# Kernel optimization log

Hardware: AMD Instinct MI355X
Metric: run time of the kernel (lower is better)

The kernel has to match this reference:

```python
import jax, jax.numpy as jnp
import numpy as np

QMIN, QMAX = -128.0, 127.0  # 8-bit signed activation range


def fq_act(x, s):
    """Fake-quantize activations: clip(round(x/s))*s with straight-through estimator."""
    y = jnp.clip(jnp.round(x / s), QMIN, QMAX) * s
    return x + jax.lax.stop_gradient(y - x)


def fq_weight(w):
    """Per-tensor max-abs symmetric (narrow-range) 8-bit weight fake-quant with STE."""
    s = jnp.max(jnp.abs(w)) / 127.0
    y = jnp.clip(jnp.round(w / s), -127.0, 127.0) * s
    return w + jax.lax.stop_gradient(y - w)


def conv1x1(x, w, b):
    # x: [b,c,h,w], w: [o,c] -> [b,o,h,w]
    return jnp.einsum('bchw,oc->bohw', x, w) + b[None, :, None, None]


def setup_inputs() -> dict:
    key = jax.random.key(0)
    ks = jax.random.split(key, 6)
    B, C, HC, H, W = 8, 64, 32, 64, 64
    x = jax.random.normal(ks[0], (B, C, H, W), dtype=jnp.float32)
    wq = jax.random.normal(ks[1], (HC, C), dtype=jnp.float32) * 0.05
    wk = jax.random.normal(ks[2], (HC, C), dtype=jnp.float32) * 0.05
    wv = jax.random.normal(ks[3], (HC, C), dtype=jnp.float32) * 0.05
    wp = jax.random.normal(ks[4], (C, HC), dtype=jnp.float32) * 0.05
    return {
        'x': x,
        'wq': wq, 'bq': jnp.zeros((HC,), jnp.float32),
        'wk': wk, 'bk': jnp.zeros((HC,), jnp.float32),
        'wv': wv, 'bv': jnp.zeros((HC,), jnp.float32),
        'wp': wp, 'bp': jnp.zeros((C,), jnp.float32),
        's_in': jnp.ones((1,), jnp.float32) * 0.0625,
        's_out': jnp.ones((1,), jnp.float32) * 0.0625,
    }


def reference(x, wq, bq, wk, bk, wv, bv, wp, bp, s_in, s_out):
    b, c, h, w = x.shape
    hc = wq.shape[0]
    n = h * w
    xq = fq_act(x, s_in)                              # quant_inp(x)
    q = conv1x1(xq, fq_weight(wq), bq).reshape(b, hc, n).transpose(0, 2, 1)  # [b,n,hc]
    k = conv1x1(xq, fq_weight(wk), bk).reshape(b, hc, n)                     # [b,hc,n]
    v = conv1x1(xq, fq_weight(wv), bv).reshape(b, hc, n).transpose(0, 2, 1)  # [b,n,hc]
    z = jax.nn.softmax(jnp.einsum('bqc,bck->bqk', q, k), axis=-1)            # [b,n,n]
    z = jnp.einsum('bqk,bkc->bqc', z, v).transpose(0, 2, 1).reshape(b, hc, h, w)
    z = fq_act(z, s_in)                               # quant_inp(z) (shared module/scale)
    out = xq + conv1x1(z, fq_weight(wp), bp)
    return fq_act(out, s_out)                         # self.act QuantIdentity
```

## Files before the change

kernel.cpp:

```cpp
#include <hip/hip_runtime.h>
#include <hip/hip_bf16.h>
#include <cstdint>
#include <cstddef>

#define NB 8
#define NC 64
#define NHC 32
#define NN 4096
#define LOG2E 1.44269504088896340736f

typedef short v8s __attribute__((ext_vector_type(8)));
typedef short v4s __attribute__((ext_vector_type(4)));
typedef float v4f __attribute__((ext_vector_type(4)));
typedef unsigned int v2u __attribute__((ext_vector_type(2)));

__device__ __forceinline__ unsigned short f2b(float f) {
    unsigned int u = __builtin_bit_cast(unsigned int, f);
    u += 0x7fffu + ((u >> 16) & 1u);
    return (unsigned short)(u >> 16);
}
__device__ __forceinline__ float b2f(unsigned short s) {
    unsigned int u = ((unsigned int)s) << 16;
    return __builtin_bit_cast(float, u);
}
__device__ __forceinline__ unsigned int pack2_bf16(float a, float b) {
    unsigned int ua = __builtin_bit_cast(unsigned int, a);
    ua += 0x7fffu + ((ua >> 16) & 1u);
    unsigned int ub = __builtin_bit_cast(unsigned int, b);
    ub += 0x7fffu + ((ub >> 16) & 1u);
    return (ua >> 16) | (ub & 0xffff0000u);
}
__device__ __forceinline__ unsigned int trunc2_bf16(float a, float b) {
    return __builtin_amdgcn_perm(__builtin_bit_cast(unsigned int, b),
                                 __builtin_bit_cast(unsigned int, a), 0x07060302u);
}
__device__ __forceinline__ float wave_max(float v) {
    #pragma unroll
    for (int off = 1; off < 64; off <<= 1) v = fmaxf(v, __shfl_xor(v, off));
    return v;
}
__device__ __forceinline__ v4f mfma16bf16(v4s a, v4s b, v4f c) {
#if __has_builtin(__builtin_amdgcn_mfma_f32_16x16x16bf16_1k)
    return __builtin_amdgcn_mfma_f32_16x16x16bf16_1k(a, b, c, 0, 0, 0);
#else
    asm volatile("v_mfma_f32_16x16x16_bf16 %0, %1, %2, %0"
                 : "+v"(c) : "v"(a), "v"(b));
    return c;
#endif
}

__global__ __launch_bounds__(256) void k_qkv(
    const float* __restrict__ x,
    const float* __restrict__ wq, const float* __restrict__ wk, const float* __restrict__ wv,
    const float* __restrict__ bq, const float* __restrict__ bk, const float* __restrict__ bv,
    const float* __restrict__ s_in,
    unsigned short* __restrict__ xqb, unsigned short* __restrict__ qb,
    unsigned short* __restrict__ kb, unsigned short* __restrict__ vb)
{
    int blk = blockIdx.x;
    int b   = blk >> 6;
    int p0  = (blk & 63) * 64;
    int tid = threadIdx.x;
    int wave = tid >> 6;
    int lane = tid & 63;

    __shared__ __align__(16) unsigned short xt[64][72];
    __shared__ __align__(16) unsigned short wlds[6144];
    __shared__ float red[3][4];

    float4 q0 = *(const float4*)(wq + tid * 8), q1 = *(const float4*)(wq + tid * 8 + 4);
    float4 k0 = *(const float4*)(wk + tid * 8), k1 = *(const float4*)(wk + tid * 8 + 4);
    float4 v0 = *(const float4*)(wv + tid * 8), v1 = *(const float4*)(wv + tid * 8 + 4);
    float mq = fmaxf(fmaxf(fmaxf(fabsf(q0.x), fabsf(q0.y)), fmaxf(fabsf(q0.z), fabsf(q0.w))),
                     fmaxf(fmaxf(fabsf(q1.x), fabsf(q1.y)), fmaxf(fabsf(q1.z), fabsf(q1.w))));
    float mk = fmaxf(fmaxf(fmaxf(fabsf(k0.x), fabsf(k0.y)), fmaxf(fabsf(k0.z), fabsf(k0.w))),
                     fmaxf(fmaxf(fabsf(k1.x), fabsf(k1.y)), fmaxf(fabsf(k1.z), fabsf(k1.w))));
    float mv = fmaxf(fmaxf(fmaxf(fabsf(v0.x), fabsf(v0.y)), fmaxf(fabsf(v0.z), fabsf(v0.w))),
                     fmaxf(fmaxf(fabsf(v1.x), fabsf(v1.y)), fmaxf(fabsf(v1.z), fabsf(v1.w))));
    mq = wave_max(mq); mk = wave_max(mk); mv = wave_max(mv);
    if (lane == 0) { red[0][wave] = mq; red[1][wave] = mk; red[2][wave] = mv; }
    __syncthreads();
    float sq = fmaxf(fmaxf(red[0][0], red[0][1]), fmaxf(red[0][2], red[0][3])) / 127.0f;
    float sk = fmaxf(fmaxf(red[1][0], red[1][1]), fmaxf(red[1][2], red[1][3])) / 127.0f;
    float sw = fmaxf(fmaxf(red[2][0], red[2][1]), fmaxf(red[2][2], red[2][3])) / 127.0f;
    {
        float eq[8] = {q0.x, q0.y, q0.z, q0.w, q1.x, q1.y, q1.z, q1.w};
        float ek[8] = {k0.x, k0.y, k0.z, k0.w, k1.x, k1.y, k1.z, k1.w};
        float ev[8] = {v0.x, v0.y, v0.z, v0.w, v1.x, v1.y, v1.z, v1.w};
        #pragma unroll
        for (int j = 0; j < 8; ++j) {
            wlds[0 * 2048 + tid * 8 + j] = f2b(fminf(fmaxf(rintf(eq[j] / sq), -127.f), 127.f) * sq);
            wlds[1 * 2048 + tid * 8 + j] = f2b(fminf(fmaxf(rintf(ek[j] / sk), -127.f), 127.f) * sk);
            wlds[2 * 2048 + tid * 8 + j] = f2b(fminf(fmaxf(rintf(ev[j] / sw), -127.f), 127.f) * sw);
        }
    }

    float sv = s_in[0];
    float sinv = 1.0f / sv;
    int jj = tid & 15;
    int c0 = tid >> 4;
    #pragma unroll
    for (int it = 0; it < 4; ++it) {
        int c = c0 + it * 16;
        size_t gi = ((size_t)(b * NC + c) << 12) + p0 + jj * 4;
        float4 xv = *(const float4*)(x + gi);
        float r0 = fminf(fmaxf(rintf(xv.x * sinv), -128.f), 127.f) * sv;
        float r1 = fminf(fmaxf(rintf(xv.y * sinv), -128.f), 127.f) * sv;
        float r2 = fminf(fmaxf(rintf(xv.z * sinv), -128.f), 127.f) * sv;
        float r3 = fminf(fmaxf(rintf(xv.w * sinv), -128.f), 127.f) * sv;
        *(uint2*)(xqb + gi) = make_uint2(pack2_bf16(r0, r1), pack2_bf16(r2, r3));
        xt[jj * 4 + 0][c] = f2b(r0);
        xt[jj * 4 + 1][c] = f2b(r1);
        xt[jj * 4 + 2][c] = f2b(r2);
        xt[jj * 4 + 3][c] = f2b(r3);
    }
    __syncthreads();

    int quad = lane >> 4;
    int l15  = lane & 15;

    v8s bf0 = *(const v8s*)(&xt[wave * 16 + l15][0  + quad * 8]);
    v8s bf1 = *(const v8s*)(&xt[wave * 16 + l15][32 + quad * 8]);

    int pos = p0 + wave * 16 + l15;
    size_t posg = (size_t)b * NN + pos;
    int posP = p0 + (l15 >> 2) * 16 + wave * 4 + (l15 & 3);
    const v4f zc = {0.f, 0.f, 0.f, 0.f};

    #pragma unroll
    for (int rb = 0; rb < 6; ++rb) {
        v8s a0 = *(const v8s*)(wlds + (rb * 16 + l15) * 64 + 0  + quad * 8);
        v8s a1 = *(const v8s*)(wlds + (rb * 16 + l15) * 64 + 32 + quad * 8);
        v4f t   = __builtin_amdgcn_mfma_f32_16x16x32_bf16(a0, bf0, zc, 0, 0, 0);
        v4f acc = __builtin_amdgcn_mfma_f32_16x16x32_bf16(a1, bf1, t, 0, 0, 0);

        int R0 = rb * 16 + quad * 4;
        float vals[4];
        #pragma unroll
        for (int r = 0; r < 4; ++r) {
            int R = R0 + r;
            float bias = (R < 32) ? bq[R] : (R < 64) ? bk[R - 32] : bv[R - 64];
            float vv = acc[r] + bias;
            if (R < 32) vv *= LOG2E;
            vals[r] = vv;
        }
        if (R0 < 32) {
            *(unsigned int*)(qb + posg * NHC + R0)     = pack2_bf16(vals[0], vals[1]);
            *(unsigned int*)(qb + posg * NHC + R0 + 2) = pack2_bf16(vals[2], vals[3]);
        } else if (R0 < 64) {
            *(unsigned int*)(kb + posg * NHC + R0 - 32)     = pack2_bf16(vals[0], vals[1]);
            *(unsigned int*)(kb + posg * NHC + R0 - 32 + 2) = pack2_bf16(vals[2], vals[3]);
        } else {
            #pragma unroll
            for (int r = 0; r < 4; ++r)
                vb[(size_t)(b * NHC + R0 - 64 + r) * NN + posP] = f2b(vals[r]);
        }
    }
}

__global__ __launch_bounds__(256, 2) void k_attn(
    const unsigned short* __restrict__ qb, const unsigned short* __restrict__ kb,
    const unsigned short* __restrict__ vb, const unsigned short* __restrict__ xqb,
    const float* __restrict__ wp, const float* __restrict__ bp,
    const float* __restrict__ s_in, const float* __restrict__ s_out,
    float* __restrict__ out)
{
    int blk  = blockIdx.x;
    int b    = blk >> 6;
    int qt   = blk & 63;
    int qbase = qt * 64;
    int tid  = threadIdx.x;
    int wave = tid >> 6;
    int lane = tid & 63;
    int quad = lane >> 4;
    int l15  = lane & 15;

    __shared__ __align__(16) float zbuf[4][64][36];
    __shared__ float lbuf[4][64];
    __shared__ __align__(16) unsigned short wpq[2048];
    __shared__ float redw[4];

    {
        float4 a0 = *(const float4*)(wp + tid * 8), a1 = *(const float4*)(wp + tid * 8 + 4);
        float mx = fmaxf(fmaxf(fmaxf(fabsf(a0.x), fabsf(a0.y)), fmaxf(fabsf(a0.z), fabsf(a0.w))),
                         fmaxf(fmaxf(fabsf(a1.x), fabsf(a1.y)), fmaxf(fabsf(a1.z), fabsf(a1.w))));
        mx = wave_max(mx);
        if (lane == 0) redw[wave] = mx;
        __syncthreads();
        float scale = fmaxf(fmaxf(redw[0], redw[1]), fmaxf(redw[2], redw[3])) / 127.0f;
        float e[8] = {a0.x, a0.y, a0.z, a0.w, a1.x, a1.y, a1.z, a1.w};
        #pragma unroll
        for (int j = 0; j < 8; ++j) {
            float r = fminf(fmaxf(rintf(e[j] / scale), -127.f), 127.f);
            wpq[tid * 8 + j] = f2b(r * scale);
        }
    }

    const unsigned short* qbat = qb + (size_t)b * NN * NHC;
    const unsigned short* kbat = kb + (size_t)b * NN * NHC;
    const unsigned short* vbat = vb + (size_t)b * NHC * NN;

    v8s qf[4];
    #pragma unroll
    for (int s = 0; s < 4; ++s)
        qf[s] = *(const v8s*)(qbat + (qbase + s * 16 + l15) * NHC + quad * 8);

    const v4f zc = {0.f, 0.f, 0.f, 0.f};
    v4f zt[4][2] = {{zc, zc}, {zc, zc}, {zc, zc}, {zc, zc}};
    float psA[4] = {0.f, 0.f, 0.f, 0.f};
    float psB[4] = {0.f, 0.f, 0.f, 0.f};

    int k0 = wave * 1024;
    const unsigned short* vrow0 = vbat + (size_t)( 0 + l15) * NN;
    const unsigned short* vrow1 = vbat + (size_t)(16 + l15) * NN;

    v8s ck0 = *(const v8s*)(kbat + (k0 +  0 + l15) * NHC + quad * 8);
    v8s ck1 = *(const v8s*)(kbat + (k0 + 16 + l15) * NHC + quad * 8);
    v8s ck2 = *(const v8s*)(kbat + (k0 + 32 + l15) * NHC + quad * 8);
    v8s ck3 = *(const v8s*)(kbat + (k0 + 48 + l15) * NHC + quad * 8);

    #pragma unroll 1
    for (int i = 0; i < 16; ++i) {
        int cki = k0 + (i << 6);
        int nki = k0 + (((i + 1) & 15) << 6);
        v8s nk0 = *(const v8s*)(kbat + (nki +  0 + l15) * NHC + quad * 8);
        v8s nk1 = *(const v8s*)(kbat + (nki + 16 + l15) * NHC + quad * 8);
        v8s nk2 = *(const v8s*)(kbat + (nki + 32 + l15) * NHC + quad * 8);
        v8s nk3 = *(const v8s*)(kbat + (nki + 48 + l15) * NHC + quad * 8);
        v8s v00 = *(const v8s*)(vrow0 + cki + quad * 16);
        v8s v01 = *(const v8s*)(vrow0 + cki + quad * 16 + 8);
        v8s v10 = *(const v8s*)(vrow1 + cki + quad * 16);
        v8s v11 = *(const v8s*)(vrow1 + cki + quad * 16 + 8);
        v4s va[2][4];
        va[0][0] = __builtin_shufflevector(v00, v00, 0, 1, 2, 3);
        va[0][1] = __builtin_shufflevector(v00, v00, 4, 5, 6, 7);
        va[0][2] = __builtin_shufflevector(v01, v01, 0, 1, 2, 3);
        va[0][3] = __builtin_shufflevector(v01, v01, 4, 5, 6, 7);
        va[1][0] = __builtin_shufflevector(v10, v10, 0, 1, 2, 3);
        va[1][1] = __builtin_shufflevector(v10, v10, 4, 5, 6, 7);
        va[1][2] = __builtin_shufflevector(v11, v11, 0, 1, 2, 3);
        va[1][3] = __builtin_shufflevector(v11, v11, 4, 5, 6, 7);

        #pragma unroll
        for (int s = 0; s < 4; ++s) {
            v4f sa[4];
            sa[0] = __builtin_amdgcn_mfma_f32_16x16x32_bf16(ck0, qf[s], zc, 0, 0, 0);
            sa[1] = __builtin_amdgcn_mfma_f32_16x16x32_bf16(ck1, qf[s], zc, 0, 0, 0);
            sa[2] = __builtin_amdgcn_mfma_f32_16x16x32_bf16(ck2, qf[s], zc, 0, 0, 0);
            sa[3] = __builtin_amdgcn_mfma_f32_16x16x32_bf16(ck3, qf[s], zc, 0, 0, 0);

            #pragma unroll
            for (int t = 0; t < 4; ++t) {
                float p0 = __builtin_amdgcn_exp2f(sa[t][0]);
                float p1 = __builtin_amdgcn_exp2f(sa[t][1]);
                float p2 = __builtin_amdgcn_exp2f(sa[t][2]);
                float p3 = __builtin_amdgcn_exp2f(sa[t][3]);
                psA[s] += p0 + p1;
                psB[s] += p2 + p3;
                v2u w;
                w.x = trunc2_bf16(p0, p1);
                w.y = trunc2_bf16(p2, p3);
                v4s pfrag = __builtin_bit_cast(v4s, w);
                zt[s][0] = mfma16bf16(va[0][t], pfrag, zt[s][0]);
                zt[s][1] = mfma16bf16(va[1][t], pfrag, zt[s][1]);
            }
        }
        ck0 = nk0; ck1 = nk1; ck2 = nk2; ck3 = nk3;
    }

    #pragma unroll
    for (int s = 0; s < 4; ++s) {
        *(v4f*)(&zbuf[wave][s * 16 + l15][     quad * 4]) = zt[s][0];
        *(v4f*)(&zbuf[wave][s * 16 + l15][16 + quad * 4]) = zt[s][1];
        float ps = psA[s] + psB[s];
        ps += __shfl_xor(ps, 16);
        ps += __shfl_xor(ps, 32);
        if (quad == 0) lbuf[wave][s * 16 + l15] = ps;
    }
    __syncthreads();

    int myq = wave * 16 + l15;
    float L = lbuf[0][myq] + lbuf[1][myq] + lbuf[2][myq] + lbuf[3][myq];

    float z[8] = {0.f};
    #pragma unroll
    for (int w = 0; w < 4; ++w) {
        v4f za  = *(const v4f*)(&zbuf[w][myq][quad * 8]);
        v4f zb2 = *(const v4f*)(&zbuf[w][myq][quad * 8 + 4]);
        #pragma unroll
        for (int j = 0; j < 4; ++j) { z[j] += za[j]; z[4 + j] += zb2[j]; }
    }
    float sv = s_in[0], sinv = 1.0f / sv;
    float so = s_out[0], soinv = 1.0f / so;
    float Linv = 1.0f / L;
    unsigned int zp[4];
    #pragma unroll
    for (int jp = 0; jp < 4; ++jp) {
        float a = z[2 * jp]     * Linv;
        float c = z[2 * jp + 1] * Linv;
        a = fminf(fmaxf(rintf(a * sinv), -128.f), 127.f) * sv;
        c = fminf(fmaxf(rintf(c * sinv), -128.f), 127.f) * sv;
        zp[jp] = pack2_bf16(a, c);
    }
    v8s zf = __builtin_bit_cast(v8s, *(uint4*)zp);

    v8s w0f = *(const v8s*)(wpq + ( 0 + l15) * NHC + quad * 8);
    v8s w1f = *(const v8s*)(wpq + (16 + l15) * NHC + quad * 8);
    v8s w2f = *(const v8s*)(wpq + (32 + l15) * NHC + quad * 8);
    v8s w3f = *(const v8s*)(wpq + (48 + l15) * NHC + quad * 8);
    v4f o0 = __builtin_amdgcn_mfma_f32_16x16x32_bf16(w0f, zf, zc, 0, 0, 0);
    v4f o1 = __builtin_amdgcn_mfma_f32_16x16x32_bf16(w1f, zf, zc, 0, 0, 0);
    v4f o2 = __builtin_amdgcn_mfma_f32_16x16x32_bf16(w2f, zf, zc, 0, 0, 0);
    v4f o3 = __builtin_amdgcn_mfma_f32_16x16x32_bf16(w3f, zf, zc, 0, 0, 0);

    int pos = qbase + wave * 16 + l15;
    #pragma unroll
    for (int ot = 0; ot < 4; ++ot) {
        v4f ov = (ot == 0) ? o0 : (ot == 1) ? o1 : (ot == 2) ? o2 : o3;
        #pragma unroll
        for (int r = 0; r < 4; ++r) {
            int oc = ot * 16 + quad * 4 + r;
            size_t idx = (size_t)(b * NC + oc) * NN + pos;
            float val = ov[r] + bp[oc] + b2f(xqb[idx]);
            float f = fminf(fmaxf(rintf(val * soinv), -128.f), 127.f);
            out[idx] = f * so;
        }
    }
}

extern "C" void kernel_launch(void* const* d_in, const int* in_sizes, int n_in,
                              void* d_out, int out_size, void* d_ws, size_t ws_size,
                              hipStream_t stream) {
    const float* x     = (const float*)d_in[0];
    const float* wq    = (const float*)d_in[1];
    const float* bq    = (const float*)d_in[2];
    const float* wk    = (const float*)d_in[3];
    const float* bk    = (const float*)d_in[4];
    const float* wv    = (const float*)d_in[5];
    const float* bv    = (const float*)d_in[6];
    const float* wp    = (const float*)d_in[7];
    const float* bp    = (const float*)d_in[8];
    const float* s_in  = (const float*)d_in[9];
    const float* s_out = (const float*)d_in[10];
    float* out = (float*)d_out;

    char* ws = (char*)d_ws;
    size_t off = 0;
    auto carve = [&](size_t bytes) {
        void* p = ws + off;
        off = (off + bytes + 255) & ~(size_t)255;
        return p;
    };
    unsigned short* xqb = (unsigned short*)carve((size_t)NB * NC * NN * 2);
    unsigned short* qbf = (unsigned short*)carve((size_t)NB * NN * NHC * 2);
    unsigned short* kbf = (unsigned short*)carve((size_t)NB * NN * NHC * 2);
    unsigned short* vbf = (unsigned short*)carve((size_t)NB * NHC * NN * 2);

    hipLaunchKernelGGL(k_qkv, dim3(512), dim3(256), 0, stream,
                       x, wq, wk, wv, bq, bk, bv, s_in, xqb, qbf, kbf, vbf);
    hipLaunchKernelGGL(k_attn, dim3(512), dim3(256), 0, stream,
                       qbf, kbf, vbf, xqb, wp, bp, s_in, s_out, out);
}
```

Baseline: 112.7 us.

## Use 16x16x32 MFMA for PV product with matching V layout and prefetch

Replaces the 16x16x16 bf16 MFMAs in the attention P·V step with 16x16x32 MFMAs that consume two score tiles at once. This halves the PV instruction count and drops the per-iteration shuffles of V fragments. The V store permutation in the QKV kernel changes so each lane's 8 contiguous keys line up with the new fragment layout. V fragments are now prefetched one iteration ahead, and s_setprio hints are added around the MFMA groups to favour matrix issue. The cost is extra registers for the double-buffered V, and correctness depends on the permuted key ordering matching exactly.

```diff
diff --git a/kernel.cpp b/kernel.cpp
--- a/kernel.cpp
+++ b/kernel.cpp
@@ -10,9 +10,8 @@
 #define LOG2E 1.44269504088896340736f
 
 typedef short v8s __attribute__((ext_vector_type(8)));
-typedef short v4s __attribute__((ext_vector_type(4)));
 typedef float v4f __attribute__((ext_vector_type(4)));
-typedef unsigned int v2u __attribute__((ext_vector_type(2)));
+typedef unsigned int v4u __attribute__((ext_vector_type(4)));
 
 __device__ __forceinline__ unsigned short f2b(float f) {
     unsigned int u = __builtin_bit_cast(unsigned int, f);
@@ -38,15 +37,6 @@
     #pragma unroll
     for (int off = 1; off < 64; off <<= 1) v = fmaxf(v, __shfl_xor(v, off));
     return v;
-}
-__device__ __forceinline__ v4f mfma16bf16(v4s a, v4s b, v4f c) {
-#if __has_builtin(__builtin_amdgcn_mfma_f32_16x16x16bf16_1k)
-    return __builtin_amdgcn_mfma_f32_16x16x16bf16_1k(a, b, c, 0, 0, 0);
-#else
-    asm volatile("v_mfma_f32_16x16x16_bf16 %0, %1, %2, %0"
-                 : "+v"(c) : "v"(a), "v"(b));
-    return c;
-#endif
 }
 
 __global__ __launch_bounds__(256) void k_qkv(
@@ -124,7 +114,7 @@
 
     int pos = p0 + wave * 16 + l15;
     size_t posg = (size_t)b * NN + pos;
-    int posP = p0 + (l15 >> 2) * 16 + wave * 4 + (l15 & 3);
+    int posP = p0 + (wave >> 1) * 32 + (l15 >> 2) * 8 + (wave & 1) * 4 + (l15 & 3);
     const v4f zc = {0.f, 0.f, 0.f, 0.f};
 
     #pragma unroll
@@ -218,54 +208,66 @@
     v8s ck1 = *(const v8s*)(kbat + (k0 + 16 + l15) * NHC + quad * 8);
     v8s ck2 = *(const v8s*)(kbat + (k0 + 32 + l15) * NHC + quad * 8);
     v8s ck3 = *(const v8s*)(kbat + (k0 + 48 + l15) * NHC + quad * 8);
+    v8s cv00 = *(const v8s*)(vrow0 + k0      + quad * 8);
+    v8s cv01 = *(const v8s*)(vrow0 + k0 + 32 + quad * 8);
+    v8s cv10 = *(const v8s*)(vrow1 + k0      + quad * 8);
+    v8s cv11 = *(const v8s*)(vrow1 + k0 + 32 + quad * 8);
 
     #pragma unroll 1
     for (int i = 0; i < 16; ++i) {
-        int cki = k0 + (i << 6);
         int nki = k0 + (((i + 1) & 15) << 6);
         v8s nk0 = *(const v8s*)(kbat + (nki +  0 + l15) * NHC + quad * 8);
         v8s nk1 = *(const v8s*)(kbat + (nki + 16 + l15) * NHC + quad * 8);
         v8s nk2 = *(const v8s*)(kbat + (nki + 32 + l15) * NHC + quad * 8);
         v8s nk3 = *(const v8s*)(kbat + (nki + 48 + l15) * NHC + quad * 8);
-        v8s v00 = *(const v8s*)(vrow0 + cki + quad * 16);
-        v8s v01 = *(const v8s*)(vrow0 + cki + quad * 16 + 8);
-        v8s v10 = *(const v8s*)(vrow1 + cki + quad * 16);
-        v8s v11 = *(const v8s*)(vrow1 + cki + quad * 16 + 8);
-        v4s va[2][4];
-        va[0][0] = __builtin_shufflevector(v00, v00, 0, 1, 2, 3);
-        va[0][1] = __builtin_shufflevector(v00, v00, 4, 5, 6, 7);
-        va[0][2] = __builtin_shufflevector(v01, v01, 0, 1, 2, 3);
-        va[0][3] = __builtin_shufflevector(v01, v01, 4, 5, 6, 7);
-        va[1][0] = __builtin_shufflevector(v10, v10, 0, 1, 2, 3);
-        va[1][1] = __builtin_shufflevector(v10, v10, 4, 5, 6, 7);
-        va[1][2] = __builtin_shufflevector(v11, v11, 0, 1, 2, 3);
-        va[1][3] = __builtin_shufflevector(v11, v11, 4, 5, 6, 7);
+        v8s nv00 = *(const v8s*)(vrow0 + nki      + quad * 8);
+        v8s nv01 = *(const v8s*)(vrow0 + nki + 32 + quad * 8);
+        v8s nv10 = *(const v8s*)(vrow1 + nki      + quad * 8);
+        v8s nv11 = *(const v8s*)(vrow1 + nki + 32 + quad * 8);
 
         #pragma unroll
         for (int s = 0; s < 4; ++s) {
             v4f sa[4];
+            __builtin_amdgcn_s_setprio(1);
             sa[0] = __builtin_amdgcn_mfma_f32_16x16x32_bf16(ck0, qf[s], zc, 0, 0, 0);
             sa[1] = __builtin_amdgcn_mfma_f32_16x16x32_bf16(ck1, qf[s], zc, 0, 0, 0);
             sa[2] = __builtin_amdgcn_mfma_f32_16x16x32_bf16(ck2, qf[s], zc, 0, 0, 0);
             sa[3] = __builtin_amdgcn_mfma_f32_16x16x32_bf16(ck3, qf[s], zc, 0, 0, 0);
+            __builtin_amdgcn_s_setprio(0);
 
             #pragma unroll
-            for (int t = 0; t < 4; ++t) {
-                float p0 = __builtin_amdgcn_exp2f(sa[t][0]);
-                float p1 = __builtin_amdgcn_exp2f(sa[t][1]);
-                float p2 = __builtin_amdgcn_exp2f(sa[t][2]);
-                float p3 = __builtin_amdgcn_exp2f(sa[t][3]);
-                psA[s] += p0 + p1;
-                psB[s] += p2 + p3;
-                v2u w;
-                w.x = trunc2_bf16(p0, p1);
-                w.y = trunc2_bf16(p2, p3);
-                v4s pfrag = __builtin_bit_cast(v4s, w);
-                zt[s][0] = mfma16bf16(va[0][t], pfrag, zt[s][0]);
-                zt[s][1] = mfma16bf16(va[1][t], pfrag, zt[s][1]);
+            for (int g = 0; g < 2; ++g) {
+                float p00 = __builtin_amdgcn_exp2f(sa[2 * g][0]);
+                float p01 = __builtin_amdgcn_exp2f(sa[2 * g][1]);
+                float p02 = __builtin_amdgcn_exp2f(sa[2 * g][2]);
+                float p03 = __builtin_amdgcn_exp2f(sa[2 * g][3]);
+                float p10 = __builtin_amdgcn_exp2f(sa[2 * g + 1][0]);
+                float p11 = __builtin_amdgcn_exp2f(sa[2 * g + 1][1]);
+                float p12 = __builtin_amdgcn_exp2f(sa[2 * g + 1][2]);
+                float p13 = __builtin_amdgcn_exp2f(sa[2 * g + 1][3]);
+                psA[s] += p00 + p01;
+                psB[s] += p02 + p03;
+                psA[s] += p10 + p11;
+                psB[s] += p12 + p13;
+                v4u w;
+                w.x = trunc2_bf16(p00, p01);
+                w.y = trunc2_bf16(p02, p03);
+                w.z = trunc2_bf16(p10, p11);
+                w.w = trunc2_bf16(p12, p13);
+                v8s pfrag = __builtin_bit_cast(v8s, w);
+                __builtin_amdgcn_s_setprio(1);
+                if (g == 0) {
+                    zt[s][0] = __builtin_amdgcn_mfma_f32_16x16x32_bf16(cv00, pfrag, zt[s][0], 0, 0, 0);
+                    zt[s][1] = __builtin_amdgcn_mfma_f32_16x16x32_bf16(cv10, pfrag, zt[s][1], 0, 0, 0);
+                } else {
+                    zt[s][0] = __builtin_amdgcn_mfma_f32_16x16x32_bf16(cv01, pfrag, zt[s][0], 0, 0, 0);
+                    zt[s][1] = __builtin_amdgcn_mfma_f32_16x16x32_bf16(cv11, pfrag, zt[s][1], 0, 0, 0);
+                }
+                __builtin_amdgcn_s_setprio(0);
             }
         }
         ck0 = nk0; ck1 = nk1; ck2 = nk2; ck3 = nk3;
+        cv00 = nv00; cv01 = nv01; cv10 = nv10; cv11 = nv11;
     }
 
     #pragma unroll
```

Measured after the change: 112.4 us. About the same (-0.3%).
